# Optimization experiments

Hardware: AMD Instinct MI355X
Metric: run time of the kernel (lower is better)

Reference implementation:

```python
import jax, jax.numpy as jnp
import numpy as np

B, S, D = 4, 8192, 1024   # batch, seq_len, d_model
DG = 256                  # genre embedding dim
E, K = 64, 2              # n_experts, top_k


def setup_inputs() -> dict:
    key = jax.random.key(0)
    k1, k2, k3, k4 = jax.random.split(key, 4)
    x = jax.random.normal(k1, (B, S, D), dtype=jnp.float32)
    genre_emb = jax.random.normal(k2, (B, DG), dtype=jnp.float32)
    # router parameters (kaiming-ish scale)
    Wx = jax.random.normal(k3, (D, E), dtype=jnp.float32) / np.sqrt(D)
    Wg = jax.random.normal(k4, (DG, E), dtype=jnp.float32) / np.sqrt(DG)
    b = jnp.zeros((E,), dtype=jnp.float32)
    return {"x": x, "genre_emb": genre_emb, "Wx": Wx, "Wg": Wg, "b": b}


def reference(x, genre_emb, Wx, Wg, b):
    # Router logits conditioned on token state and broadcast genre embedding.
    # x: [B,S,D], genre_emb: [B,DG] -> logits [B,S,E]
    logits = jnp.einsum("bsd,de->bse", x, Wx) + (genre_emb @ Wg)[:, None, :] + b
    probs = jax.nn.softmax(logits, axis=-1)          # [B,S,E]
    topk_vals, topk_idx = jax.lax.top_k(probs, K)    # [B,S,K]
    # renormalize selected expert weights to sum to 1
    topk_vals = topk_vals / topk_vals.sum(axis=-1, keepdims=True)
    # scatter back to sparse dense gate tensor [B,S,E]
    onehot = jax.nn.one_hot(topk_idx, E, dtype=topk_vals.dtype)  # [B,S,K,E]
    gates = jnp.einsum("bsk,bske->bse", topk_vals, onehot)
    return gates, topk_idx
```

## Files before the change

### kernel.cpp

```cpp
#include <hip/hip_runtime.h>
#include <math.h>

#define NTOK   32768
#define DMODEL 1024
#define NEXP   64
#define DGENRE 256
#define BK     64
#define TT     64

typedef const __attribute__((address_space(1))) void ga_void;
typedef __attribute__((address_space(3))) void lds_void;

__device__ __forceinline__ bool better(float va, int ia, float vb, int ib) {
  return (va > vb) || (va == vb && ia < ib);
}

__global__ __launch_bounds__(256, 2) void moe_gate_k(
    const float* __restrict__ x, const float* __restrict__ Wx,
    const float* __restrict__ genre, const float* __restrict__ Wg,
    const float* __restrict__ bias, float* __restrict__ out) {
  __shared__ __align__(16) float xs[2][TT * BK];
  __shared__ __align__(16) float ws[2][BK * NEXP];
  __shared__ float cpart[4][NEXP];
  __shared__ float cbias[NEXP];

  const int tid  = threadIdx.x;
  const int wv   = tid >> 6;
  const int lane = tid & 63;
  const int tok0 = blockIdx.x * TT;
  const int b    = tok0 >> 13;

  {
    const int e = tid & 63, dc = tid >> 6;
    const float* g  = genre + b * DGENRE + dc * 64;
    const float* wg = Wg + (size_t)(dc * 64) * NEXP + e;
    float p = 0.f;
#pragma unroll 8
    for (int d = 0; d < 64; ++d) p = fmaf(g[d], wg[(size_t)d * NEXP], p);
    cpart[dc][e] = p;
  }

  const int eg = tid & 15;
  const int tg = tid >> 4;
  const int e0 = eg * 4;
  const int t0 = tg * 4;
  const int sw = tg & 3;

  float acc[4][4] = {{0.f}};

#define STAGE(bufidx, d0)                                                      \
  {                                                                            \
    _Pragma("unroll")                                                          \
    for (int s = 0; s < 4; ++s) {                                              \
      const int L = wv * 256 + s * 64 + lane;                                  \
      const int t = L >> 4, pq = L & 15;                                       \
      const int dq = pq ^ ((t >> 2) & 3);                                      \
      const float* gsrc = x + (size_t)(tok0 + t) * DMODEL + (d0) + dq * 4;     \
      __builtin_amdgcn_global_load_lds((ga_void*)gsrc,                         \
          (lds_void*)&xs[bufidx][(wv * 256 + s * 64) * 4], 16, 0, 0);          \
      const float* wsrc = Wx + (size_t)(d0) * NEXP + L * 4;                    \
      __builtin_amdgcn_global_load_lds((ga_void*)wsrc,                         \
          (lds_void*)&ws[bufidx][(wv * 256 + s * 64) * 4], 16, 0, 0);          \
    }                                                                          \
  }

#define COMPUTE(bufidx)                                                        \
  {                                                                            \
    const float* xb = &xs[bufidx][0];                                          \
    const float* wb = &ws[bufidx][0];                                          \
    _Pragma("unroll 4")                                                        \
    for (int dq = 0; dq < 16; ++dq) {                                          \
      float4 xv[4], wv4[4];                                                    \
      _Pragma("unroll")                                                        \
      for (int i = 0; i < 4; ++i)                                              \
        xv[i] = *reinterpret_cast<const float4*>(                              \
            &xb[(t0 + i) * BK + ((dq ^ sw) << 2)]);                            \
      _Pragma("unroll")                                                        \
      for (int dd = 0; dd < 4; ++dd)                                           \
        wv4[dd] = *reinterpret_cast<const float4*>(                            \
            &wb[(dq * 4 + dd) * NEXP + e0]);                                   \
      _Pragma("unroll")                                                        \
      for (int dd = 0; dd < 4; ++dd) {                                         \
        _Pragma("unroll")                                                      \
        for (int i = 0; i < 4; ++i) {                                          \
          const float xvv = reinterpret_cast<const float*>(&xv[i])[dd];        \
          _Pragma("unroll")                                                    \
          for (int j = 0; j < 4; ++j)                                          \
            acc[i][j] = fmaf(                                                  \
                xvv, reinterpret_cast<const float*>(&wv4[dd])[j], acc[i][j]);  \
        }                                                                      \
      }                                                                        \
    }                                                                          \
  }

  STAGE(0, 0);
  __syncthreads();
  if (tid < NEXP)
    cbias[tid] = bias[tid] + cpart[0][tid] + cpart[1][tid] + cpart[2][tid] +
                 cpart[3][tid];

  for (int c = 0; c < DMODEL / BK; ++c) {
    if (c < DMODEL / BK - 1) STAGE((c + 1) & 1, (c + 1) * BK);
    COMPUTE(c & 1);
    __syncthreads();
  }

#pragma unroll
  for (int j = 0; j < 4; ++j) {
    const float cb = cbias[e0 + j];
#pragma unroll
    for (int i = 0; i < 4; ++i) acc[i][j] += cb;
  }

  float* gates  = out;
  float* idxout = out + (size_t)NTOK * NEXP;

#pragma unroll
  for (int i = 0; i < 4; ++i) {
    float v1 = acc[i][0]; int i1 = e0;
    float v2 = -INFINITY; int i2 = NEXP;
#pragma unroll
    for (int j = 1; j < 4; ++j) {
      const float a = acc[i][j]; const int ei = e0 + j;
      if (better(a, ei, v1, i1)) { v2 = v1; i2 = i1; v1 = a; i1 = ei; }
      else if (better(a, ei, v2, i2)) { v2 = a; i2 = ei; }
    }
#pragma unroll
    for (int m = 1; m < 16; m <<= 1) {
      const float ov1 = __shfl_xor(v1, m, 64); const int oi1 = __shfl_xor(i1, m, 64);
      const float ov2 = __shfl_xor(v2, m, 64); const int oi2 = __shfl_xor(i2, m, 64);
      if (better(v1, i1, ov1, oi1)) {
        if (better(ov1, oi1, v2, i2)) { v2 = ov1; i2 = oi1; }
      } else {
        if (better(v1, i1, ov2, oi2)) { v2 = v1; i2 = i1; }
        else                          { v2 = ov2; i2 = oi2; }
        v1 = ov1; i1 = oi1;
      }
    }
    const float ew  = expf(v2 - v1);
    const float inv = 1.0f / (1.0f + ew);
    const float w1 = inv, w2 = ew * inv;

    const int tok = tok0 + t0 + i;
    float4 g;
    g.x = (e0 + 0 == i1) ? w1 : ((e0 + 0 == i2) ? w2 : 0.0f);
    g.y = (e0 + 1 == i1) ? w1 : ((e0 + 1 == i2) ? w2 : 0.0f);
    g.z = (e0 + 2 == i1) ? w1 : ((e0 + 2 == i2) ? w2 : 0.0f);
    g.w = (e0 + 3 == i1) ? w1 : ((e0 + 3 == i2) ? w2 : 0.0f);
    *reinterpret_cast<float4*>(&gates[(size_t)tok * NEXP + e0]) = g;

    if (eg == 0) {
      idxout[(size_t)tok * 2 + 0] = (float)i1;
      idxout[(size_t)tok * 2 + 1] = (float)i2;
    }
  }
}

extern "C" void kernel_launch(void* const* d_in, const int* in_sizes, int n_in,
                              void* d_out, int out_size, void* d_ws, size_t ws_size,
                              hipStream_t stream) {
  const float* x     = (const float*)d_in[0];
  const float* genre = (const float*)d_in[1];
  const float* Wx    = (const float*)d_in[2];
  const float* Wg    = (const float*)d_in[3];
  const float* bias  = (const float*)d_in[4];
  float* out = (float*)d_out;

  moe_gate_k<<<NTOK / TT, 256, 0, stream>>>(x, Wx, genre, Wg, bias, out);
}
```

Before: 222.6 us.

## Split K across waves with 8x8 register tiles and LDS cross-wave reduction

Each thread now accumulates a full 8-token by 8-expert tile instead of 4x4. Each of the four waves handles one quarter of every 64-wide K chunk, and the partial sums are combined through shared memory at the end. The x and Wx staging swizzles are reworked so that the wider float4 reads hit banks without conflicts. The goal is to raise the ratio of FMAs to LDS reads, which looks like the main bottleneck. In exchange it adds a multi-step reduction with extra barriers, leaves top-k and the output store to wave 0 alone, and raises register pressure.

```diff
diff --git a/kernel.cpp b/kernel.cpp
--- a/kernel.cpp
+++ b/kernel.cpp
@@ -7,6 +7,7 @@
 #define DGENRE 256
 #define BK     64
 #define TT     64
+#define NCHUNK (DMODEL / BK)
 
 typedef const __attribute__((address_space(1))) void ga_void;
 typedef __attribute__((address_space(3))) void lds_void;
@@ -19,14 +20,16 @@
     const float* __restrict__ x, const float* __restrict__ Wx,
     const float* __restrict__ genre, const float* __restrict__ Wg,
     const float* __restrict__ bias, float* __restrict__ out) {
-  __shared__ __align__(16) float xs[2][TT * BK];
-  __shared__ __align__(16) float ws[2][BK * NEXP];
+  __shared__ __align__(16) float smem[16384];
   __shared__ float cpart[4][NEXP];
   __shared__ float cbias[NEXP];
 
   const int tid  = threadIdx.x;
-  const int wv   = tid >> 6;
   const int lane = tid & 63;
+  const int wv   = __builtin_amdgcn_readfirstlane(tid >> 6);
+  const int tg   = lane >> 3;
+  const int eg   = lane & 7;
+  const int e0   = eg * 8;
   const int tok0 = blockIdx.x * TT;
   const int b    = tok0 >> 13;
 
@@ -40,54 +43,60 @@
     cpart[dc][e] = p;
   }
 
-  const int eg = tid & 15;
-  const int tg = tid >> 4;
-  const int e0 = eg * 4;
-  const int t0 = tg * 4;
-  const int sw = tg & 3;
-
-  float acc[4][4] = {{0.f}};
+  float acc[8][8];
+#pragma unroll
+  for (int i = 0; i < 8; ++i)
+#pragma unroll
+    for (int j = 0; j < 8; ++j) acc[i][j] = 0.f;
 
 #define STAGE(bufidx, d0)                                                      \
   {                                                                            \
     _Pragma("unroll")                                                          \
     for (int s = 0; s < 4; ++s) {                                              \
-      const int L = wv * 256 + s * 64 + lane;                                  \
-      const int t = L >> 4, pq = L & 15;                                       \
-      const int dq = pq ^ ((t >> 2) & 3);                                      \
-      const float* gsrc = x + (size_t)(tok0 + t) * DMODEL + (d0) + dq * 4;     \
-      __builtin_amdgcn_global_load_lds((ga_void*)gsrc,                         \
-          (lds_void*)&xs[bufidx][(wv * 256 + s * 64) * 4], 16, 0, 0);          \
-      const float* wsrc = Wx + (size_t)(d0) * NEXP + L * 4;                    \
-      __builtin_amdgcn_global_load_lds((ga_void*)wsrc,                         \
-          (lds_void*)&ws[bufidx][(wv * 256 + s * 64) * 4], 16, 0, 0);          \
+      const int S = s * 256 + tid;                                             \
+      const int t = S >> 4, q = S & 15;                                        \
+      const int dq = q ^ ((t >> 3) & 7);                                       \
+      const float* gx = x + (size_t)(tok0 + t) * DMODEL + (d0) + dq * 4;       \
+      __builtin_amdgcn_global_load_lds((ga_void*)gx,                           \
+          (lds_void*)&smem[(bufidx) * 4096 + (s * 256 + wv * 64) * 4],         \
+          16, 0, 0);                                                           \
+      const int qe = ((q & 7) << 1) | (q >> 3);                                \
+      const float* gw = Wx + (size_t)((d0) + t) * NEXP + qe * 4;               \
+      __builtin_amdgcn_global_load_lds((ga_void*)gw,                           \
+          (lds_void*)&smem[8192 + (bufidx) * 4096 + (s * 256 + wv * 64) * 4],  \
+          16, 0, 0);                                                           \
     }                                                                          \
   }
 
 #define COMPUTE(bufidx)                                                        \
   {                                                                            \
-    const float* xb = &xs[bufidx][0];                                          \
-    const float* wb = &ws[bufidx][0];                                          \
-    _Pragma("unroll 4")                                                        \
-    for (int dq = 0; dq < 16; ++dq) {                                          \
-      float4 xv[4], wv4[4];                                                    \
+    const float* xb = &smem[(bufidx) * 4096];                                  \
+    const float* wb = &smem[8192 + (bufidx) * 4096];                           \
+    _Pragma("unroll")                                                          \
+    for (int dq = 0; dq < 4; ++dq) {                                           \
+      const int Q = wv * 4 + dq;                                               \
+      float4 xv[8];                                                            \
       _Pragma("unroll")                                                        \
-      for (int i = 0; i < 4; ++i)                                              \
+      for (int i = 0; i < 8; ++i)                                              \
         xv[i] = *reinterpret_cast<const float4*>(                              \
-            &xb[(t0 + i) * BK + ((dq ^ sw) << 2)]);                            \
-      _Pragma("unroll")                                                        \
-      for (int dd = 0; dd < 4; ++dd)                                           \
-        wv4[dd] = *reinterpret_cast<const float4*>(                            \
-            &wb[(dq * 4 + dd) * NEXP + e0]);                                   \
+            &xb[(tg * 8 + i) * 64 + ((Q ^ tg) << 2)]);                         \
       _Pragma("unroll")                                                        \
       for (int dd = 0; dd < 4; ++dd) {                                         \
+        const int d = Q * 4 + dd;                                              \
+        const float4 w0 = *reinterpret_cast<const float4*>(                    \
+            &wb[d * 64 + eg * 4]);                                             \
+        const float4 w1 = *reinterpret_cast<const float4*>(                    \
+            &wb[d * 64 + 32 + eg * 4]);                                        \
+        const float* wa0 = reinterpret_cast<const float*>(&w0);                \
+        const float* wa1 = reinterpret_cast<const float*>(&w1);                \
         _Pragma("unroll")                                                      \
-        for (int i = 0; i < 4; ++i) {                                          \
-          const float xvv = reinterpret_cast<const float*>(&xv[i])[dd];        \
+        for (int i = 0; i < 8; ++i) {                                          \
+          const float xd = reinterpret_cast<const float*>(&xv[i])[dd];         \
           _Pragma("unroll")                                                    \
-          for (int j = 0; j < 4; ++j)                                          \
-            acc[i][j] = fmaf(                                                  \
-                xvv, reinterpret_cast<const float*>(&wv4[dd])[j], acc[i][j]);  \
+          for (int j = 0; j < 4; ++j) {                                        \
+            acc[i][j]     = fmaf(xd, wa0[j], acc[i][j]);                       \
+            acc[i][j + 4] = fmaf(xd, wa1[j], acc[i][j + 4]);                   \
+          }                                                                    \
         }                                                                      \
       }                                                                        \
     }                                                                          \
@@ -99,59 +108,101 @@
     cbias[tid] = bias[tid] + cpart[0][tid] + cpart[1][tid] + cpart[2][tid] +
                  cpart[3][tid];
 
-  for (int c = 0; c < DMODEL / BK; ++c) {
-    if (c < DMODEL / BK - 1) STAGE((c + 1) & 1, (c + 1) * BK);
+  for (int c = 0; c < NCHUNK; ++c) {
+    if (c < NCHUNK - 1) STAGE((c + 1) & 1, (c + 1) * BK);
     COMPUTE(c & 1);
     __syncthreads();
   }
 
-#pragma unroll
-  for (int j = 0; j < 4; ++j) {
-    const float cb = cbias[e0 + j];
-#pragma unroll
-    for (int i = 0; i < 4; ++i) acc[i][j] += cb;
-  }
-
-  float* gates  = out;
-  float* idxout = out + (size_t)NTOK * NEXP;
-
-#pragma unroll
-  for (int i = 0; i < 4; ++i) {
-    float v1 = acc[i][0]; int i1 = e0;
-    float v2 = -INFINITY; int i2 = NEXP;
-#pragma unroll
-    for (int j = 1; j < 4; ++j) {
-      const float a = acc[i][j]; const int ei = e0 + j;
-      if (better(a, ei, v1, i1)) { v2 = v1; i2 = i1; v1 = a; i1 = ei; }
-      else if (better(a, ei, v2, i2)) { v2 = a; i2 = ei; }
-    }
-#pragma unroll
-    for (int m = 1; m < 16; m <<= 1) {
-      const float ov1 = __shfl_xor(v1, m, 64); const int oi1 = __shfl_xor(i1, m, 64);
-      const float ov2 = __shfl_xor(v2, m, 64); const int oi2 = __shfl_xor(i2, m, 64);
-      if (better(v1, i1, ov1, oi1)) {
-        if (better(ov1, oi1, v2, i2)) { v2 = ov1; i2 = oi1; }
-      } else {
-        if (better(v1, i1, ov2, oi2)) { v2 = v1; i2 = i1; }
-        else                          { v2 = ov2; i2 = oi2; }
-        v1 = ov1; i1 = oi1;
-      }
-    }
-    const float ew  = expf(v2 - v1);
-    const float inv = 1.0f / (1.0f + ew);
-    const float w1 = inv, w2 = ew * inv;
-
-    const int tok = tok0 + t0 + i;
-    float4 g;
-    g.x = (e0 + 0 == i1) ? w1 : ((e0 + 0 == i2) ? w2 : 0.0f);
-    g.y = (e0 + 1 == i1) ? w1 : ((e0 + 1 == i2) ? w2 : 0.0f);
-    g.z = (e0 + 2 == i1) ? w1 : ((e0 + 2 == i2) ? w2 : 0.0f);
-    g.w = (e0 + 3 == i1) ? w1 : ((e0 + 3 == i2) ? w2 : 0.0f);
-    *reinterpret_cast<float4*>(&gates[(size_t)tok * NEXP + e0]) = g;
-
-    if (eg == 0) {
-      idxout[(size_t)tok * 2 + 0] = (float)i1;
-      idxout[(size_t)tok * 2 + 1] = (float)i2;
+  if (wv >= 2) {
+    float* r = &smem[(wv - 2) * 4352 + lane * 68];
+#pragma unroll
+    for (int i = 0; i < 8; ++i) {
+      float4 t0 = {acc[i][0], acc[i][1], acc[i][2], acc[i][3]};
+      float4 t1 = {acc[i][4], acc[i][5], acc[i][6], acc[i][7]};
+      *reinterpret_cast<float4*>(&r[i * 8])     = t0;
+      *reinterpret_cast<float4*>(&r[i * 8 + 4]) = t1;
+    }
+  }
+  __syncthreads();
+  if (wv < 2) {
+    const float* r = &smem[wv * 4352 + lane * 68];
+#pragma unroll
+    for (int i = 0; i < 8; ++i) {
+      float4 t0 = *reinterpret_cast<const float4*>(&r[i * 8]);
+      float4 t1 = *reinterpret_cast<const float4*>(&r[i * 8 + 4]);
+      acc[i][0] += t0.x; acc[i][1] += t0.y; acc[i][2] += t0.z; acc[i][3] += t0.w;
+      acc[i][4] += t1.x; acc[i][5] += t1.y; acc[i][6] += t1.z; acc[i][7] += t1.w;
+    }
+  }
+  __syncthreads();
+  if (wv == 1) {
+    float* r = &smem[lane * 68];
+#pragma unroll
+    for (int i = 0; i < 8; ++i) {
+      float4 t0 = {acc[i][0], acc[i][1], acc[i][2], acc[i][3]};
+      float4 t1 = {acc[i][4], acc[i][5], acc[i][6], acc[i][7]};
+      *reinterpret_cast<float4*>(&r[i * 8])     = t0;
+      *reinterpret_cast<float4*>(&r[i * 8 + 4]) = t1;
+    }
+  }
+  __syncthreads();
+
+  if (wv == 0) {
+    const float* r = &smem[lane * 68];
+    float* gates  = out;
+    float* idxout = out + (size_t)NTOK * NEXP;
+
+#pragma unroll
+    for (int i = 0; i < 8; ++i) {
+      float4 t0 = *reinterpret_cast<const float4*>(&r[i * 8]);
+      float4 t1 = *reinterpret_cast<const float4*>(&r[i * 8 + 4]);
+      acc[i][0] += t0.x; acc[i][1] += t0.y; acc[i][2] += t0.z; acc[i][3] += t0.w;
+      acc[i][4] += t1.x; acc[i][5] += t1.y; acc[i][6] += t1.z; acc[i][7] += t1.w;
+#pragma unroll
+      for (int j = 0; j < 8; ++j) acc[i][j] += cbias[e0 + j];
+
+      float v1 = acc[i][0]; int i1 = e0;
+      float v2 = -INFINITY; int i2 = NEXP;
+#pragma unroll
+      for (int j = 1; j < 8; ++j) {
+        const float a = acc[i][j]; const int ei = e0 + j;
+        if (better(a, ei, v1, i1)) { v2 = v1; i2 = i1; v1 = a; i1 = ei; }
+        else if (better(a, ei, v2, i2)) { v2 = a; i2 = ei; }
+      }
+#pragma unroll
+      for (int m = 1; m < 8; m <<= 1) {
+        const float ov1 = __shfl_xor(v1, m, 64); const int oi1 = __shfl_xor(i1, m, 64);
+        const float ov2 = __shfl_xor(v2, m, 64); const int oi2 = __shfl_xor(i2, m, 64);
+        if (better(v1, i1, ov1, oi1)) {
+          if (better(ov1, oi1, v2, i2)) { v2 = ov1; i2 = oi1; }
+        } else {
+          if (better(v1, i1, ov2, oi2)) { v2 = v1; i2 = i1; }
+          else                          { v2 = ov2; i2 = oi2; }
+          v1 = ov1; i1 = oi1;
+        }
+      }
+      const float ew  = expf(v2 - v1);
+      const float inv = 1.0f / (1.0f + ew);
+      const float w1 = inv, w2 = ew * inv;
+
+      const int tok = tok0 + tg * 8 + i;
+      float4 g0, g1;
+      float* gp0 = reinterpret_cast<float*>(&g0);
+      float* gp1 = reinterpret_cast<float*>(&g1);
+#pragma unroll
+      for (int k = 0; k < 4; ++k) {
+        const int ea = e0 + k, eb = e0 + 4 + k;
+        gp0[k] = (ea == i1) ? w1 : ((ea == i2) ? w2 : 0.0f);
+        gp1[k] = (eb == i1) ? w1 : ((eb == i2) ? w2 : 0.0f);
+      }
+      *reinterpret_cast<float4*>(&gates[(size_t)tok * NEXP + e0])     = g0;
+      *reinterpret_cast<float4*>(&gates[(size_t)tok * NEXP + e0 + 4]) = g1;
+
+      if (eg == 0) {
+        idxout[(size_t)tok * 2 + 0] = (float)i1;
+        idxout[(size_t)tok * 2 + 1] = (float)i2;
+      }
     }
   }
 }
```

After: 229.5 us. 1.03x slower.
